# Kernel optimization log

Hardware: AMD Instinct MI355X
Metric: run time of the kernel (lower is better)

The kernel has to match this reference:

```python
import jax, jax.numpy as jnp
import numpy as np

B, NQ, NK, C = 16, 8, 4096, 256
H = W = 64
HEADS = 8
CI = 128          # embedding_dim // attention_downsample_rate
HD = CI // HEADS  # per-head dim
EPS = float(np.finfo(np.float32).tiny)


def _gumbel_topk(scores, noise, n):
    # iterative gumbel-softmax top-k relaxation with straight-through hard k-hot
    g = scores + noise
    khot = jnp.zeros_like(g)
    onehot = jnp.zeros_like(g)
    for _ in range(n):
        g = g + jnp.log(jnp.maximum(1.0 - onehot, EPS))
        onehot = jax.nn.softmax(g, axis=-1)
        khot = khot + onehot
    _, ind = jax.lax.top_k(khot, n)
    rows = jnp.arange(khot.shape[0])[:, None]
    hard = jnp.zeros_like(khot).at[rows, ind].set(1.0)
    ret = hard - jax.lax.stop_gradient(khot) + khot  # == hard numerically
    return ret, jnp.sort(ind, axis=1)  # sorted idx = row-major order of boolean-mask select


def _sample_points(pe, content, ret, idx):
    # pe [H,W,C], content [b,H,W,C], ret [b,HW] k-hot, idx [b,k] sorted
    b = ret.shape[0]
    m = ret.reshape(b, H, W, 1)
    pe_m = (pe[None] * m).reshape(b, H * W, -1)
    c_m = (content * m).reshape(b, H * W, -1)
    take = lambda a: jnp.take_along_axis(a, idx[:, :, None], axis=1)
    return take(pe_m), take(c_m)


def _mlp(x, W1, b1, W2, b2, W3, b3):
    x = jax.nn.relu(x @ W1 + b1)
    x = jax.nn.relu(x @ W2 + b2)
    return x @ W3 + b3


def _forward(queries, keys, query_pe, key_pe, guiding_embedding, gumbel_p, gumbel_n,
             static_uncertain, static_refined, Wq, bq, Wk, bk, Wv, bv, Wo, bo,
             uW1, ub1, uW2, ub2, uW3, ub3, rW1, rb1, rW2, rb2, rW3, rb3,
             pe_gauss, point_pos, point_neg, n_sample_points):
    b = queries.shape[0]
    g = guiding_embedding.reshape(b, C, H * W).transpose(0, 2, 1)  # [b, HW, C]
    g = g * keys  # elementwise gating -> new guiding embedding

    # cross attention token -> image (internal dim CI, HEADS heads)
    def split_heads(x, Wx, bx):
        return (x @ Wx + bx).reshape(b, -1, HEADS, HD).transpose(0, 2, 1, 3)
    qh = split_heads(queries + query_pe, Wq, bq)
    kh = split_heads(g + key_pe, Wk, bk)
    vh = split_heads(g, Wv, bv)
    attn = jax.nn.softmax(jnp.einsum('bhqd,bhkd->bhqk', qh, kh) / np.float32(np.sqrt(HD)), axis=-1)
    out = jnp.einsum('bhqk,bhkd->bhqd', attn, vh).transpose(0, 2, 1, 3).reshape(b, -1, CI)
    queries = out @ Wo + bo  # [b, NQ, C]

    q1 = queries[:, 1, :]
    unc_tok = _mlp(jnp.concatenate([jnp.broadcast_to(static_uncertain, (b, C)), q1], -1),
                   uW1, ub1, uW2, ub2, uW3, ub3)
    ref_tok = _mlp(jnp.concatenate([jnp.broadcast_to(static_refined, (b, C)), q1], -1),
                   rW1, rb1, rW2, rb2, rW3, rb3)

    img = g.transpose(0, 2, 1)  # [b, C, HW]
    unc_norm = jax.nn.sigmoid(jnp.einsum('bc,bcn->bn', unc_tok, img))
    ref_mask = jnp.einsum('bc,bcn->bn', ref_tok, img)
    coarse_mask = jnp.einsum('bc,bcn->bn', q1, img)

    queries = jnp.concatenate([queries[:, 0:1], ref_tok[:, None, :], queries[:, 2:]], axis=1)

    # point-sampling reference map + gumbel-softmax top-k (training-path math)
    ref_map = unc_norm * (jax.nn.sigmoid(ref_mask) - jax.nn.sigmoid(coarse_mask))  # [b, HW]
    ret_p, idx_p = _gumbel_topk(ref_map, gumbel_p, n_sample_points)
    ret_n, idx_n = _gumbel_topk(-ref_map, gumbel_n, n_sample_points)

    # random fourier positional encoding of the 64x64 grid (SAM PositionEmbeddingRandom)
    xs = (jnp.arange(W, dtype=jnp.float32) + 0.5) / W
    ys = (jnp.arange(H, dtype=jnp.float32) + 0.5) / H
    coords = jnp.stack([jnp.tile(xs[None, :], (H, 1)), jnp.tile(ys[:, None], (1, W))], axis=-1)
    proj = ((2.0 * coords - 1.0) @ pe_gauss) * np.float32(2.0 * np.pi)  # [H, W, C//2]
    pe = jnp.concatenate([jnp.sin(proj), jnp.cos(proj)], axis=-1)       # [H, W, C]

    # F.interpolate of a 64x64 map to (64,64) is the identity here
    content = (keys + g).reshape(b, H, W, C)

    sp_pe, sp_c = _sample_points(pe, content, ret_p, idx_p)
    sn_pe, sn_c = _sample_points(pe, content, ret_n, idx_n)
    sp_pe = sp_pe + point_pos  # prompt_encoder.point_embeddings[1]
    sn_pe = sn_pe + point_neg  # prompt_encoder.point_embeddings[0]

    query_pe = jnp.concatenate([query_pe, sp_pe, sn_pe], axis=1)
    queries = jnp.concatenate([queries, sp_c, sn_c], axis=1)
    # pack (queries, query_pe) into one array for a single-output reference
    return jnp.concatenate([queries, query_pe], axis=1)  # [b, 2*(NQ+2k), C]


def setup_inputs():
    key = jax.random.key(0)
    ks = iter(jax.random.split(key, 48))
    n = lambda shape, s=1.0: jax.random.normal(next(ks), shape, jnp.float32) * s
    z = lambda shape: jnp.zeros(shape, jnp.float32)
    return {
        'queries': n((B, NQ, C)),
        'keys': n((B, NK, C)),
        'query_pe': n((B, NQ, C)),
        'key_pe': n((B, NK, C)),
        'guiding_embedding': n((B, C, H, W)),
        'gumbel_p': jax.random.gumbel(next(ks), (B, NK), jnp.float32),
        'gumbel_n': jax.random.gumbel(next(ks), (B, NK), jnp.float32),
        'static_uncertain': n((C,), 0.02),
        'static_refined': n((C,), 0.02),
        'Wq': n((C, CI), 0.02), 'bq': z((CI,)),
        'Wk': n((C, CI), 0.02), 'bk': z((CI,)),
        'Wv': n((C, CI), 0.02), 'bv': z((CI,)),
        'Wo': n((CI, C), 0.02), 'bo': z((C,)),
        'uW1': n((2 * C, C // 4), 0.05), 'ub1': z((C // 4,)),
        'uW2': n((C // 4, C // 4), 0.05), 'ub2': z((C // 4,)),
        'uW3': n((C // 4, C), 0.05), 'ub3': z((C,)),
        'rW1': n((2 * C, C // 4), 0.05), 'rb1': z((C // 4,)),
        'rW2': n((C // 4, C // 4), 0.05), 'rb2': z((C // 4,)),
        'rW3': n((C // 4, C), 0.05), 'rb3': z((C,)),
        'pe_gauss': n((2, C // 2)),
        'point_pos': n((C,), 0.02),
        'point_neg': n((C,), 0.02),
        'n_sample_points': 4,
    }


def reference(queries, keys, query_pe, key_pe, guiding_embedding, gumbel_p, gumbel_n,
              static_uncertain, static_refined, Wq, bq, Wk, bk, Wv, bv, Wo, bo,
              uW1, ub1, uW2, ub2, uW3, ub3, rW1, rb1, rW2, rb2, rW3, rb3,
              pe_gauss, point_pos, point_neg, n_sample_points):
    return _forward(queries, keys, query_pe, key_pe, guiding_embedding, gumbel_p, gumbel_n,
                    static_uncertain, static_refined, Wq, bq, Wk, bk, Wv, bv, Wo, bo,
                    uW1, ub1, uW2, ub2, uW3, ub3, rW1, rb1, rW2, rb2, rW3, rb3,
                    pe_gauss, point_pos, point_neg, n_sample_points)
```

## Files before the change

### kernel.cpp

```cpp
#include <hip/hip_runtime.h>

#define BB 16
#define NQn 8
#define NK 4096
#define CC 256
#define NHEADS 8
#define CIn 128
#define HDn 16
#define NHQ 64
#define EPS_TINY 1.17549435e-38f

constexpr size_t OFF_QK   = 0;
constexpr size_t OFF_QBK  = OFF_QK  + (size_t)BB*CC*NHQ;
constexpr size_t OFF_SC   = OFF_QBK + (size_t)BB*NHQ;
constexpr size_t OFF_MP   = OFF_SC  + (size_t)BB*NK*NHQ;
constexpr size_t OFF_SP   = OFF_MP  + (size_t)BB*16*NHQ;
constexpr size_t OFF_M    = OFF_SP  + (size_t)BB*16*NHQ;
constexpr size_t OFF_RS   = OFF_M   + (size_t)BB*NHQ;
constexpr size_t OFF_AVP  = OFF_RS  + (size_t)BB*NHQ;
constexpr size_t OFF_QATT = OFF_AVP + (size_t)BB*16*NHQ*CC;
constexpr size_t OFF_UNC  = OFF_QATT+ (size_t)BB*NQn*CC;
constexpr size_t OFF_REFT = OFF_UNC + (size_t)BB*CC;
constexpr size_t OFF_RMAP = OFF_REFT+ (size_t)BB*CC;
constexpr size_t OFF_IDX  = OFF_RMAP+ (size_t)BB*NK;
constexpr size_t OFF_RV   = OFF_IDX + 128;
constexpr size_t OFF_G    = OFF_RV  + 128;

__global__ __launch_bounds__(256) void k1_qside(
    const float* __restrict__ queries, const float* __restrict__ query_pe,
    const float* __restrict__ Wq, const float* __restrict__ bq,
    const float* __restrict__ Wk, const float* __restrict__ bk,
    float* __restrict__ ws)
{
  int b = blockIdx.x >> 3, q = blockIdx.x & 7, t = threadIdx.x;
  __shared__ float x[CC];
  __shared__ float qh[CIn];
  x[t] = queries[(b*NQn+q)*CC + t] + query_pe[(b*NQn+q)*CC + t];
  __syncthreads();
  if (t < CIn) {
    float a = bq[t];
    for (int c = 0; c < CC; ++c) a += x[c]*Wq[c*CIn + t];
    qh[t] = a * 0.25f;
  }
  __syncthreads();
  float* Qk = ws + OFF_QK;
  #pragma unroll
  for (int h = 0; h < NHEADS; ++h) {
    float a = 0.f;
    #pragma unroll
    for (int d = 0; d < HDn; ++d) a += qh[h*HDn+d] * Wk[t*CIn + h*HDn + d];
    Qk[((size_t)b*CC + t)*NHQ + h*NQn + q] = a;
  }
  if (t < NHEADS) {
    float a = 0.f;
    #pragma unroll
    for (int d = 0; d < HDn; ++d) a += qh[t*HDn+d] * bk[t*HDn+d];
    (ws + OFF_QBK)[b*NHQ + t*NQn + q] = a;
  }
}

__global__ __launch_bounds__(256) void k2_scores(
    const float* __restrict__ keys, const float* __restrict__ key_pe,
    const float* __restrict__ guiding, float* __restrict__ ws)
{
  int b = blockIdx.y, n0 = blockIdx.x * 64, t = threadIdx.x;
  __shared__ __align__(16) float Xs[64][68];
  __shared__ __align__(16) float Qs[64][64];
  __shared__ float Gt[64][65];
  const float* Qk = ws + OFF_QK;
  float* G = ws + OFF_G;
  int tx = t & 15, ty = t >> 4;
  int c4 = tx*4, rowg = ty;
  int lane = t & 63, grp = t >> 6;
  float acc[4][4] = {};

  float gpref[16];
  float4 kpref[4], ppref[4];
  float qpref[16];
  #pragma unroll
  for (int cc = 0; cc < 16; ++cc)
    gpref[cc] = guiding[((size_t)b*CC + grp*16+cc)*NK + n0 + lane];
  #pragma unroll
  for (int p = 0; p < 4; ++p) {
    size_t base = ((size_t)b*NK + n0 + p*16+rowg)*CC + c4;
    kpref[p] = *(const float4*)&keys[base];
    ppref[p] = *(const float4*)&key_pe[base];
  }
  #pragma unroll
  for (int i = 0; i < 16; ++i) {
    int l = i*256 + t;
    qpref[i] = Qk[((size_t)b*CC + (l>>6))*NHQ + (l & 63)];
  }

  for (int c0 = 0; c0 < CC; c0 += 64) {
    #pragma unroll
    for (int cc = 0; cc < 16; ++cc) Gt[grp*16+cc][lane] = gpref[cc];
    __syncthreads();
    #pragma unroll
    for (int i = 0; i < 16; ++i) {
      int l = i*256 + t;
      Qs[l >> 6][l & 63] = qpref[i];
    }
    #pragma unroll
    for (int p = 0; p < 4; ++p) {
      int row = p*16 + rowg;
      size_t base = ((size_t)b*NK + n0 + row)*CC + c0 + c4;
      float4 kv = kpref[p], pv = ppref[p];
      float4 g4;
      g4.x = kv.x * Gt[c4+0][row];
      g4.y = kv.y * Gt[c4+1][row];
      g4.z = kv.z * Gt[c4+2][row];
      g4.w = kv.w * Gt[c4+3][row];
      *(float4*)&G[base] = g4;
      float4 o; o.x = g4.x+pv.x; o.y = g4.y+pv.y; o.z = g4.z+pv.z; o.w = g4.w+pv.w;
      *(float4*)&Xs[row][c4] = o;
    }
    __syncthreads();
    if (c0 + 64 < CC) {
      int c1 = c0 + 64;
      #pragma unroll
      for (int cc = 0; cc < 16; ++cc)
        gpref[cc] = guiding[((size_t)b*CC + c1 + grp*16+cc)*NK + n0 + lane];
      #pragma unroll
      for (int p = 0; p < 4; ++p) {
        size_t base = ((size_t)b*NK + n0 + p*16+rowg)*CC + c1 + c4;
        kpref[p] = *(const float4*)&keys[base];
        ppref[p] = *(const float4*)&key_pe[base];
      }
      #pragma unroll
      for (int i = 0; i < 16; ++i) {
        int l = i*256 + t;
        qpref[i] = Qk[((size_t)b*CC + c1 + (l>>6))*NHQ + (l & 63)];
      }
    }
    #pragma unroll 4
    for (int cb = 0; cb < 16; ++cb) {
      float4 xf[4], qf[4];
      #pragma unroll
      for (int i = 0; i < 4; ++i) xf[i] = *(const float4*)&Xs[4*ty+i][4*cb];
      #pragma unroll
      for (int u = 0; u < 4; ++u) qf[u] = *(const float4*)&Qs[4*cb+u][4*tx];
      #pragma unroll
      for (int u = 0; u < 4; ++u) {
        float xu[4] = { ((const float*)&xf[0])[u], ((const float*)&xf[1])[u],
                        ((const float*)&xf[2])[u], ((const float*)&xf[3])[u] };
        float qu[4] = { qf[u].x, qf[u].y, qf[u].z, qf[u].w };
        #pragma unroll
        for (int i = 0; i < 4; ++i)
          #pragma unroll
          for (int j = 0; j < 4; ++j) acc[i][j] += xu[i]*qu[j];
      }
    }
  }
  const float* qbk = ws + OFF_QBK + (size_t)b*NHQ;
  float qb[4] = {qbk[4*tx], qbk[4*tx+1], qbk[4*tx+2], qbk[4*tx+3]};
  float* sc = ws + OFF_SC + ((size_t)b*NK + n0)*NHQ;
  #pragma unroll
  for (int i = 0; i < 4; ++i) {
    float4 o;
    o.x = acc[i][0]+qb[0]; o.y = acc[i][1]+qb[1]; o.z = acc[i][2]+qb[2]; o.w = acc[i][3]+qb[3];
    *(float4*)&sc[(4*ty + i)*NHQ + 4*tx] = o;
  }
}

__global__ __launch_bounds__(256) void k3a_stats(float* __restrict__ ws)
{
  int b = blockIdx.y, sb = blockIdx.x, t = threadIdx.x;
  int hq = t & 63, r = t >> 6;
  const float* sc = ws + OFF_SC + ((size_t)b*NK + sb*256)*NHQ;
  float m = -INFINITY, s = 0.f;
  for (int i = 0; i < 64; ++i) {
    float v = sc[(r + 4*i)*NHQ + hq];
    if (v > m) { s = s*expf(m - v) + 1.f; m = v; } else { s += expf(v - m); }
  }
  __shared__ float rm[256], rs[256];
  rm[t] = m; rs[t] = s;
  __syncthreads();
  if (t < 64) {
    float m0=rm[t], m1=rm[t+64], m2=rm[t+128], m3=rm[t+192];
    float mm = fmaxf(fmaxf(m0,m1), fmaxf(m2,m3));
    float ss = rs[t]*expf(m0-mm) + rs[t+64]*expf(m1-mm) + rs[t+128]*expf(m2-mm) + rs[t+192]*expf(m3-mm);
    (ws + OFF_MP)[(b*16 + sb)*NHQ + t] = mm;
    (ws + OFF_SP)[(b*16 + sb)*NHQ + t] = ss;
  }
}

__global__ __launch_bounds__(64) void k3b_combine(float* __restrict__ ws)
{
  int b = blockIdx.x, hq = threadIdx.x;
  const float* mp = ws + OFF_MP + (size_t)b*16*NHQ;
  const float* sp = ws + OFF_SP + (size_t)b*16*NHQ;
  float m = -INFINITY;
  #pragma unroll
  for (int i = 0; i < 16; ++i) m = fmaxf(m, mp[i*NHQ+hq]);
  float s = 0.f;
  #pragma unroll
  for (int i = 0; i < 16; ++i) s += sp[i*NHQ+hq]*expf(mp[i*NHQ+hq]-m);
  (ws+OFF_M)[b*NHQ+hq] = m;
  (ws+OFF_RS)[b*NHQ+hq] = 1.0f/s;
}

__global__ __launch_bounds__(512) void k4_av(float* __restrict__ ws)
{
  int b = blockIdx.y, kb = blockIdx.x, t = threadIdx.x;
  int k0 = kb * 256;
  __shared__ __align__(16) float gld[32][260];
  __shared__ __align__(16) float wld[32][64];
  __shared__ float mv[64], rv[64];
  if (t < 64) { mv[t] = (ws+OFF_M)[b*NHQ+t]; rv[t] = (ws+OFF_RS)[b*NHQ+t]; }
  int hq0 = (t & 7) * 8, c0 = (t >> 3) * 4;
  float accf[8][4] = {};
  const float* sc = ws + OFF_SC;
  const float* G  = ws + OFF_G;
  float4 gpref[4]; float spref[4];
  #pragma unroll
  for (int p = 0; p < 4; ++p) {
    int row = p*8 + (t>>6);
    gpref[p] = *(const float4*)&G[((size_t)b*NK + k0 + row)*CC + (t&63)*4];
  }
  #pragma unroll
  for (int i = 0; i < 4; ++i) {
    int l = i*512 + t;
    spref[i] = sc[((size_t)b*NK + k0 + (l>>6))*NHQ + (l&63)];
  }
  __syncthreads();
  for (int kk = 0; kk < 256; kk += 32) {
    #pragma unroll
    for (int p = 0; p < 4; ++p) {
      int row = p*8 + (t>>6);
      *(float4*)&gld[row][(t&63)*4] = gpref[p];
    }
    #pragma unroll
    for (int i = 0; i < 4; ++i) {
      int l = i*512 + t; int k = l >> 6, hq = l & 63;
      wld[k][hq] = expf(spref[i] - mv[hq]) * rv[hq];
    }
    __syncthreads();
    if (kk + 32 < 256) {
      #pragma unroll
      for (int p = 0; p < 4; ++p) {
        int row = p*8 + (t>>6);
        gpref[p] = *(const float4*)&G[((size_t)b*NK + k0 + kk+32 + row)*CC + (t&63)*4];
      }
      #pragma unroll
      for (int i = 0; i < 4; ++i) {
        int l = i*512 + t;
        spref[i] = sc[((size_t)b*NK + k0 + kk+32 + (l>>6))*NHQ + (l&63)];
      }
    }
    #pragma unroll 2
    for (int k = 0; k < 32; ++k) {
      float4 w0 = *(const float4*)&wld[k][hq0];
      float4 w1 = *(const float4*)&wld[k][hq0+4];
      float4 gv = *(const float4*)&gld[k][c0];
      float wq[8] = {w0.x,w0.y,w0.z,w0.w, w1.x,w1.y,w1.z,w1.w};
      float gq[4] = {gv.x,gv.y,gv.z,gv.w};
      #pragma unroll
      for (int i = 0; i < 8; ++i)
        #pragma unroll
        for (int j = 0; j < 4; ++j) accf[i][j] += wq[i]*gq[j];
    }
    __syncthreads();
  }
  float* avp = ws + OFF_AVP + (((size_t)b*16 + kb)*NHQ)*CC;
  #pragma unroll
  for (int i = 0; i < 8; ++i) {
    float4 o;
    o.x = accf[i][0]; o.y = accf[i][1]; o.z = accf[i][2]; o.w = accf[i][3];
    *(float4*)&avp[(size_t)(hq0 + i)*CC + c0] = o;
  }
}

__global__ __launch_bounds__(256) void k56_attout(
    const float* __restrict__ Wv, const float* __restrict__ bv,
    const float* __restrict__ Wo, const float* __restrict__ bo,
    float* __restrict__ ws)
{
  int b = blockIdx.x >> 3, q = blockIdx.x & 7, t = threadIdx.x;
  __shared__ float avs[NHEADS][CC];
  __shared__ float outv[CIn];
  const float* avp = ws + OFF_AVP;
  #pragma unroll
  for (int h = 0; h < NHEADS; ++h) {
    int hq = h*NQn + q;
    float a = 0.f;
    #pragma unroll 4
    for (int kb = 0; kb < 16; ++kb)
      a += avp[(((size_t)b*16 + kb)*NHQ + hq)*CC + t];
    avs[h][t] = a;
  }
  __syncthreads();
  if (t < CIn) {
    int h = t >> 4;
    float a = bv[t];
    for (int c = 0; c < CC; ++c) a += avs[h][c]*Wv[c*CIn + t];
    outv[t] = a;
  }
  __syncthreads();
  float a = bo[t];
  for (int ci = 0; ci < CIn; ++ci) a += outv[ci]*Wo[ci*CC + t];
  (ws+OFF_QATT)[((size_t)b*NQn + q)*CC + t] = a;
}

__global__ __launch_bounds__(256) void k7_mlps(
    const float* __restrict__ su, const float* __restrict__ sr,
    const float* __restrict__ uW1, const float* __restrict__ ub1,
    const float* __restrict__ uW2, const float* __restrict__ ub2,
    const float* __restrict__ uW3, const float* __restrict__ ub3,
    const float* __restrict__ rW1, const float* __restrict__ rb1,
    const float* __restrict__ rW2, const float* __restrict__ rb2,
    const float* __restrict__ rW3, const float* __restrict__ rb3,
    float* __restrict__ ws)
{
  int b = blockIdx.x, t = threadIdx.x;
  __shared__ float xs[768];
  __shared__ float h1[2][64], h2[2][64];
  xs[t] = su[t];
  xs[256+t] = (ws+OFF_QATT)[((size_t)b*NQn + 1)*CC + t];
  xs[512+t] = sr[t];
  __syncthreads();
  if (t < 128) {
    int which = t >> 6, o = t & 63;
    const float* W1 = which ? rW1 : uW1;
    const float* b1 = which ? rb1 : ub1;
    int base = which ? 512 : 0;
    float a = b1[o];
    for (int i = 0; i < 256; ++i) a += xs[base+i]*W1[i*64 + o];
    for (int i = 0; i < 256; ++i) a += xs[256+i]*W1[(256+i)*64 + o];
    h1[which][o] = fmaxf(a, 0.f);
  }
  __syncthreads();
  if (t < 128) {
    int which = t >> 6, o = t & 63;
    const float* W2 = which ? rW2 : uW2;
    const float* b2 = which ? rb2 : ub2;
    float a = b2[o];
    #pragma unroll 8
    for (int i = 0; i < 64; ++i) a += h1[which][i]*W2[i*64+o];
    h2[which][o] = fmaxf(a, 0.f);
  }
  __syncthreads();
  {
    float a = ub3[t];
    #pragma unroll 8
    for (int i = 0; i < 64; ++i) a += h2[0][i]*uW3[i*CC + t];
    (ws+OFF_UNC)[b*CC + t] = a;
    float a2 = rb3[t];
    #pragma unroll 8
    for (int i = 0; i < 64; ++i) a2 += h2[1][i]*rW3[i*CC + t];
    (ws+OFF_REFT)[b*CC + t] = a2;
  }
}

__global__ __launch_bounds__(256) void k8_masks(float* __restrict__ ws)
{
  int b = blockIdx.y, t = threadIdx.x;
  int wave = t >> 6, lane = t & 63;
  __shared__ float q1s[CC], us[CC], rts[CC];
  q1s[t] = (ws+OFF_QATT)[((size_t)b*NQn+1)*CC + t];
  us[t]  = (ws+OFF_UNC)[b*CC + t];
  rts[t] = (ws+OFF_REFT)[b*CC + t];
  __syncthreads();
  float q1v[4], usv[4], rtv[4];
  #pragma unroll
  for (int u = 0; u < 4; ++u) {
    q1v[u] = q1s[lane*4+u]; usv[u] = us[lane*4+u]; rtv[u] = rts[lane*4+u];
  }
  const float* G = ws + OFF_G;
  float* rmap = ws + OFF_RMAP + (size_t)b*NK;
  int n_base = blockIdx.x*64 + wave*16;
  for (int r = 0; r < 16; ++r) {
    int n = n_base + r;
    float4 gv = *(const float4*)&G[((size_t)b*NK + n)*CC + lane*4];
    float aq = gv.x*q1v[0] + gv.y*q1v[1] + gv.z*q1v[2] + gv.w*q1v[3];
    float au = gv.x*usv[0] + gv.y*usv[1] + gv.z*usv[2] + gv.w*usv[3];
    float ar = gv.x*rtv[0] + gv.y*rtv[1] + gv.z*rtv[2] + gv.w*rtv[3];
    #pragma unroll
    for (int s = 1; s < 64; s <<= 1) {
      aq += __shfl_xor(aq, s, 64);
      au += __shfl_xor(au, s, 64);
      ar += __shfl_xor(ar, s, 64);
    }
    if (lane == 0) {
      float un = 1.f/(1.f+expf(-au));
      rmap[n] = un * (1.f/(1.f+expf(-ar)) - 1.f/(1.f+expf(-aq)));
    }
  }
}

__global__ __launch_bounds__(256) void k9_gumbel(
    const float* __restrict__ gp, const float* __restrict__ gn,
    float* __restrict__ ws)
{
  int sign = blockIdx.x, b = blockIdx.y, t = threadIdx.x;
  int wave = t >> 6, lane = t & 63;
  const float* noise = sign ? gn : gp;
  const float* rmap = ws + OFF_RMAP + (size_t)b*NK;
  float g[16], kh[16], oh[16];
  #pragma unroll
  for (int i = 0; i < 16; ++i) {
    int n = i*256 + t;
    float scv = rmap[n];
    if (sign) scv = -scv;
    g[i] = scv + noise[(size_t)b*NK + n];
    kh[i] = 0.f; oh[i] = 0.f;
  }
  __shared__ float wred[8];
  __shared__ float selV[16];
  __shared__ int   selIdx[16];
  for (int it = 0; it < 4; ++it) {
    if (it > 0) {
      #pragma unroll
      for (int i = 0; i < 16; ++i) g[i] += logf(fmaxf(1.f - oh[i], EPS_TINY));
    }
    float m = g[0];
    #pragma unroll
    for (int i = 1; i < 16; ++i) m = fmaxf(m, g[i]);
    #pragma unroll
    for (int s = 1; s < 64; s <<= 1) m = fmaxf(m, __shfl_xor(m, s, 64));
    if (lane == 0) wred[wave] = m;
    __syncthreads();
    m = fmaxf(fmaxf(wred[0], wred[1]), fmaxf(wred[2], wred[3]));
    float e[16], ls = 0.f;
    #pragma unroll
    for (int i = 0; i < 16; ++i) { e[i] = expf(g[i]-m); ls += e[i]; }
    #pragma unroll
    for (int s = 1; s < 64; s <<= 1) ls += __shfl_xor(ls, s, 64);
    if (lane == 0) wred[4+wave] = ls;
    __syncthreads();
    float ssum = wred[4]+wred[5]+wred[6]+wred[7];
    #pragma unroll
    for (int i = 0; i < 16; ++i) { oh[i] = e[i]/ssum; kh[i] += oh[i]; }
  }
  int id[4]; float rr[4];
  for (int j = 0; j < 4; ++j) {
    float bv = kh[0]; int bi = t;
    #pragma unroll
    for (int i = 1; i < 16; ++i) {
      if (kh[i] > bv) { bv = kh[i]; bi = i*256 + t; }
    }
    #pragma unroll
    for (int s = 1; s < 64; s <<= 1) {
      float ov = __shfl_xor(bv, s, 64);
      int   oi = __shfl_xor(bi, s, 64);
      if (ov > bv || (ov == bv && oi < bi)) { bv = ov; bi = oi; }
    }
    if (lane == 0) { selV[j*4+wave] = bv; selIdx[j*4+wave] = bi; }
    __syncthreads();
    bv = selV[j*4]; bi = selIdx[j*4];
    #pragma unroll
    for (int w = 1; w < 4; ++w) {
      float ov = selV[j*4+w]; int oi = selIdx[j*4+w];
      if (ov > bv || (ov == bv && oi < bi)) { bv = ov; bi = oi; }
    }
    id[j] = bi; rr[j] = (1.f - bv) + bv;
    if ((bi & 255) == t) kh[bi >> 8] = -1.f;
  }
  if (t == 0) {
    for (int a = 0; a < 3; ++a)
      for (int c2 = a+1; c2 < 4; ++c2)
        if (id[c2] < id[a]) { int ti=id[a]; id[a]=id[c2]; id[c2]=ti; float tr=rr[a]; rr[a]=rr[c2]; rr[c2]=tr; }
    int* iout = (int*)(ws + OFF_IDX);
    float* rout = ws + OFF_RV;
    for (int j = 0; j < 4; ++j) {
      iout[(sign*BB + b)*4 + j] = id[j];
      rout[(sign*BB + b)*4 + j] = rr[j];
    }
  }
}

__global__ __launch_bounds__(256) void k10_out(
    const float* __restrict__ keys, const float* __restrict__ query_pe,
    const float* __restrict__ point_pos, const float* __restrict__ point_neg,
    const float* __restrict__ pe_gauss,
    float* __restrict__ ws, float* __restrict__ out)
{
  int b = blockIdx.y, r = blockIdx.x, t = threadIdx.x;
  const float* G = ws + OFF_G;
  float val;
  if (r < 8) {
    val = (r == 1) ? (ws+OFF_REFT)[b*CC + t]
                   : (ws+OFF_QATT)[((size_t)b*NQn + r)*CC + t];
  } else if (r < 16) {
    int j = r - 8; int sign = j >> 2; int jj = j & 3;
    int idx = ((const int*)(ws+OFF_IDX))[(sign*BB + b)*4 + jj];
    float rvv = (ws+OFF_RV)[(sign*BB + b)*4 + jj];
    float kv = keys[((size_t)b*NK + idx)*CC + t];
    float gv = G[((size_t)b*NK + idx)*CC + t];
    val = (kv + gv) * rvv;
  } else if (r < 24) {
    val = query_pe[((size_t)b*NQn + (r-16))*CC + t];
  } else {
    int j = r - 24; int sign = j >> 2; int jj = j & 3;
    int idx = ((const int*)(ws+OFF_IDX))[(sign*BB + b)*4 + jj];
    float rvv = (ws+OFF_RV)[(sign*BB + b)*4 + jj];
    const float* point = sign ? point_neg : point_pos;
    int h = idx >> 6, w = idx & 63;
    float x = (w + 0.5f)/64.f, y = (h + 0.5f)/64.f;
    int jf = (t < 128) ? t : (t - 128);
    float proj = ((2.f*x - 1.f)*pe_gauss[jf] + (2.f*y - 1.f)*pe_gauss[128 + jf]) * 6.28318530717958647692f;
    float sv = (t < 128) ? sinf(proj) : cosf(proj);
    val = sv*rvv + point[t];
  }
  out[((size_t)b*32 + r)*CC + t] = val;
}

extern "C" void kernel_launch(void* const* d_in, const int* in_sizes, int n_in,
                              void* d_out, int out_size, void* d_ws, size_t ws_size,
                              hipStream_t stream)
{
  const float* queries   = (const float*)d_in[0];
  const float* keys      = (const float*)d_in[1];
  const float* query_pe  = (const float*)d_in[2];
  const float* key_pe    = (const float*)d_in[3];
  const float* guiding   = (const float*)d_in[4];
  const float* gumbel_p  = (const float*)d_in[5];
  const float* gumbel_n  = (const float*)d_in[6];
  const float* s_unc     = (const float*)d_in[7];
  const float* s_ref     = (const float*)d_in[8];
  const float* Wq  = (const float*)d_in[9];   const float* bq  = (const float*)d_in[10];
  const float* Wk  = (const float*)d_in[11];  const float* bk  = (const float*)d_in[12];
  const float* Wv  = (const float*)d_in[13];  const float* bv  = (const float*)d_in[14];
  const float* Wo  = (const float*)d_in[15];  const float* bo  = (const float*)d_in[16];
  const float* uW1 = (const float*)d_in[17];  const float* ub1 = (const float*)d_in[18];
  const float* uW2 = (const float*)d_in[19];  const float* ub2 = (const float*)d_in[20];
  const float* uW3 = (const float*)d_in[21];  const float* ub3 = (const float*)d_in[22];
  const float* rW1 = (const float*)d_in[23];  const float* rb1 = (const float*)d_in[24];
  const float* rW2 = (const float*)d_in[25];  const float* rb2 = (const float*)d_in[26];
  const float* rW3 = (const float*)d_in[27];  const float* rb3 = (const float*)d_in[28];
  const float* pe_gauss  = (const float*)d_in[29];
  const float* point_pos = (const float*)d_in[30];
  const float* point_neg = (const float*)d_in[31];
  float* ws = (float*)d_ws;
  float* out = (float*)d_out;

  k1_qside  <<<dim3(BB*NQn),  256, 0, stream>>>(queries, query_pe, Wq, bq, Wk, bk, ws);
  k2_scores <<<dim3(64, BB),  256, 0, stream>>>(keys, key_pe, guiding, ws);
  k3a_stats <<<dim3(16, BB),  256, 0, stream>>>(ws);
  k3b_combine<<<dim3(BB),      64, 0, stream>>>(ws);
  k4_av     <<<dim3(16, BB),  512, 0, stream>>>(ws);
  k56_attout<<<dim3(BB*NQn),  256, 0, stream>>>(Wv, bv, Wo, bo, ws);
  k7_mlps   <<<dim3(BB),      256, 0, stream>>>(s_unc, s_ref, uW1, ub1, uW2, ub2, uW3, ub3,
                                                rW1, rb1, rW2, rb2, rW3, rb3, ws);
  k8_masks  <<<dim3(64, BB),  256, 0, stream>>>(ws);
  k9_gumbel <<<dim3(2, BB),   256, 0, stream>>>(gumbel_p, gumbel_n, ws);
  k10_out   <<<dim3(32, BB),  256, 0, stream>>>(keys, query_pe, point_pos, point_neg,
                                                pe_gauss, ws, out);
}
```

Baseline: 243.3 us.

## Drop k2 register prefetch and Q smem tile; split k4 across channel halves

In k2_scores, the register-level software prefetch of guiding, keys, key_pe and Qk is removed. The Qs shared tile is dropped and Qk is read directly from global memory (L1/L2) inside the inner product loop, which shrinks LDS use and register pressure at the cost of exposed load latency. In k4_av, the grid gains a channel-half dimension so each block handles 128 channels with a 4x4 register tile instead of 8x4. This doubles the block count for more occupancy and parallelism but reloads the score tiles twice.

Measured after the change: 330.3 us. 35.7% more time.

```diff
diff --git a/kernel.cpp b/kernel.cpp
--- a/kernel.cpp
+++ b/kernel.cpp
@@ -64,48 +64,29 @@
     const float* __restrict__ guiding, float* __restrict__ ws)
 {
   int b = blockIdx.y, n0 = blockIdx.x * 64, t = threadIdx.x;
-  __shared__ __align__(16) float Xs[64][68];
-  __shared__ __align__(16) float Qs[64][64];
+  __shared__ __align__(16) float Xs[64][66];
   __shared__ float Gt[64][65];
-  const float* Qk = ws + OFF_QK;
+  const float* Qk = ws + OFF_QK + (size_t)b*CC*NHQ;
   float* G = ws + OFF_G;
   int tx = t & 15, ty = t >> 4;
   int c4 = tx*4, rowg = ty;
   int lane = t & 63, grp = t >> 6;
   float acc[4][4] = {};
 
-  float gpref[16];
-  float4 kpref[4], ppref[4];
-  float qpref[16];
-  #pragma unroll
-  for (int cc = 0; cc < 16; ++cc)
-    gpref[cc] = guiding[((size_t)b*CC + grp*16+cc)*NK + n0 + lane];
-  #pragma unroll
-  for (int p = 0; p < 4; ++p) {
-    size_t base = ((size_t)b*NK + n0 + p*16+rowg)*CC + c4;
-    kpref[p] = *(const float4*)&keys[base];
-    ppref[p] = *(const float4*)&key_pe[base];
-  }
-  #pragma unroll
-  for (int i = 0; i < 16; ++i) {
-    int l = i*256 + t;
-    qpref[i] = Qk[((size_t)b*CC + (l>>6))*NHQ + (l & 63)];
-  }
-
   for (int c0 = 0; c0 < CC; c0 += 64) {
-    #pragma unroll
-    for (int cc = 0; cc < 16; ++cc) Gt[grp*16+cc][lane] = gpref[cc];
-    __syncthreads();
-    #pragma unroll
-    for (int i = 0; i < 16; ++i) {
-      int l = i*256 + t;
-      Qs[l >> 6][l & 63] = qpref[i];
-    }
+    __syncthreads();
+    #pragma unroll
+    for (int cc = 0; cc < 16; ++cc) {
+      int c = grp*16 + cc;
+      Gt[c][lane] = guiding[((size_t)b*CC + c0 + c)*NK + n0 + lane];
+    }
+    __syncthreads();
     #pragma unroll
     for (int p = 0; p < 4; ++p) {
       int row = p*16 + rowg;
       size_t base = ((size_t)b*NK + n0 + row)*CC + c0 + c4;
-      float4 kv = kpref[p], pv = ppref[p];
+      float4 kv = *(const float4*)&keys[base];
+      float4 pv = *(const float4*)&key_pe[base];
       float4 g4;
       g4.x = kv.x * Gt[c4+0][row];
       g4.y = kv.y * Gt[c4+1][row];
@@ -116,35 +97,17 @@
       *(float4*)&Xs[row][c4] = o;
     }
     __syncthreads();
-    if (c0 + 64 < CC) {
-      int c1 = c0 + 64;
-      #pragma unroll
-      for (int cc = 0; cc < 16; ++cc)
-        gpref[cc] = guiding[((size_t)b*CC + c1 + grp*16+cc)*NK + n0 + lane];
-      #pragma unroll
-      for (int p = 0; p < 4; ++p) {
-        size_t base = ((size_t)b*NK + n0 + p*16+rowg)*CC + c1 + c4;
-        kpref[p] = *(const float4*)&keys[base];
-        ppref[p] = *(const float4*)&key_pe[base];
-      }
-      #pragma unroll
-      for (int i = 0; i < 16; ++i) {
-        int l = i*256 + t;
-        qpref[i] = Qk[((size_t)b*CC + c1 + (l>>6))*NHQ + (l & 63)];
-      }
-    }
     #pragma unroll 4
     for (int cb = 0; cb < 16; ++cb) {
-      float4 xf[4], qf[4];
+      float4 xf[4];
       #pragma unroll
       for (int i = 0; i < 4; ++i) xf[i] = *(const float4*)&Xs[4*ty+i][4*cb];
       #pragma unroll
-      for (int u = 0; u < 4; ++u) qf[u] = *(const float4*)&Qs[4*cb+u][4*tx];
-      #pragma unroll
       for (int u = 0; u < 4; ++u) {
+        float4 qf = *(const float4*)&Qk[(size_t)(c0 + 4*cb + u)*NHQ + 4*tx];
         float xu[4] = { ((const float*)&xf[0])[u], ((const float*)&xf[1])[u],
                         ((const float*)&xf[2])[u], ((const float*)&xf[3])[u] };
-        float qu[4] = { qf[u].x, qf[u].y, qf[u].z, qf[u].w };
+        float qu[4] = { qf.x, qf.y, qf.z, qf.w };
         #pragma unroll
         for (int i = 0; i < 4; ++i)
           #pragma unroll
@@ -202,22 +165,21 @@
 
 __global__ __launch_bounds__(512) void k4_av(float* __restrict__ ws)
 {
-  int b = blockIdx.y, kb = blockIdx.x, t = threadIdx.x;
-  int k0 = kb * 256;
-  __shared__ __align__(16) float gld[32][260];
+  int kb = blockIdx.x, ch = blockIdx.y, b = blockIdx.z, t = threadIdx.x;
+  int k0 = kb * 256, cbase = ch * 128;
+  __shared__ __align__(16) float gld[32][132];
   __shared__ __align__(16) float wld[32][64];
   __shared__ float mv[64], rv[64];
   if (t < 64) { mv[t] = (ws+OFF_M)[b*NHQ+t]; rv[t] = (ws+OFF_RS)[b*NHQ+t]; }
-  int hq0 = (t & 7) * 8, c0 = (t >> 3) * 4;
-  float accf[8][4] = {};
+  int hq0 = (t & 15) * 4, c0 = (t >> 4) * 4;
+  int srow = t >> 5, sc4 = (t & 31) * 4;
+  float accf[4][4] = {};
   const float* sc = ws + OFF_SC;
   const float* G  = ws + OFF_G;
-  float4 gpref[4]; float spref[4];
-  #pragma unroll
-  for (int p = 0; p < 4; ++p) {
-    int row = p*8 + (t>>6);
-    gpref[p] = *(const float4*)&G[((size_t)b*NK + k0 + row)*CC + (t&63)*4];
-  }
+  float4 gpref[2]; float spref[4];
+  #pragma unroll
+  for (int p = 0; p < 2; ++p)
+    gpref[p] = *(const float4*)&G[((size_t)b*NK + k0 + p*16 + srow)*CC + cbase + sc4];
   #pragma unroll
   for (int i = 0; i < 4; ++i) {
     int l = i*512 + t;
@@ -226,10 +188,8 @@
   __syncthreads();
   for (int kk = 0; kk < 256; kk += 32) {
     #pragma unroll
-    for (int p = 0; p < 4; ++p) {
-      int row = p*8 + (t>>6);
-      *(float4*)&gld[row][(t&63)*4] = gpref[p];
-    }
+    for (int p = 0; p < 2; ++p)
+      *(float4*)&gld[p*16 + srow][sc4] = gpref[p];
     #pragma unroll
     for (int i = 0; i < 4; ++i) {
       int l = i*512 + t; int k = l >> 6, hq = l & 63;
@@ -238,25 +198,22 @@
     __syncthreads();
     if (kk + 32 < 256) {
       #pragma unroll
-      for (int p = 0; p < 4; ++p) {
-        int row = p*8 + (t>>6);
-        gpref[p] = *(const float4*)&G[((size_t)b*NK + k0 + kk+32 + row)*CC + (t&63)*4];
-      }
+      for (int p = 0; p < 2; ++p)
+        gpref[p] = *(const float4*)&G[((size_t)b*NK + k0 + kk+32 + p*16 + srow)*CC + cbase + sc4];
       #pragma unroll
       for (int i = 0; i < 4; ++i) {
         int l = i*512 + t;
         spref[i] = sc[((size_t)b*NK + k0 + kk+32 + (l>>6))*NHQ + (l&63)];
       }
     }
-    #pragma unroll 2
+    #pragma unroll 4
     for (int k = 0; k < 32; ++k) {
-      float4 w0 = *(const float4*)&wld[k][hq0];
-      float4 w1 = *(const float4*)&wld[k][hq0+4];
+      float4 w4 = *(const float4*)&wld[k][hq0];
       float4 gv = *(const float4*)&gld[k][c0];
-      float wq[8] = {w0.x,w0.y,w0.z,w0.w, w1.x,w1.y,w1.z,w1.w};
-      float gq[4] = {gv.x,gv.y,gv.z,gv.w};
+      float wq[4] = {w4.x, w4.y, w4.z, w4.w};
+      float gq[4] = {gv.x, gv.y, gv.z, gv.w};
       #pragma unroll
-      for (int i = 0; i < 8; ++i)
+      for (int i = 0; i < 4; ++i)
         #pragma unroll
         for (int j = 0; j < 4; ++j) accf[i][j] += wq[i]*gq[j];
     }
@@ -264,10 +221,10 @@
   }
   float* avp = ws + OFF_AVP + (((size_t)b*16 + kb)*NHQ)*CC;
   #pragma unroll
-  for (int i = 0; i < 8; ++i) {
+  for (int i = 0; i < 4; ++i) {
     float4 o;
     o.x = accf[i][0]; o.y = accf[i][1]; o.z = accf[i][2]; o.w = accf[i][3];
-    *(float4*)&avp[(size_t)(hq0 + i)*CC + c0] = o;
+    *(float4*)&avp[(size_t)(hq0 + i)*CC + cbase + c0] = o;
   }
 }
 
@@ -534,16 +491,16 @@
   float* ws = (float*)d_ws;
   float* out = (float*)d_out;
 
-  k1_qside  <<<dim3(BB*NQn),  256, 0, stream>>>(queries, query_pe, Wq, bq, Wk, bk, ws);
-  k2_scores <<<dim3(64, BB),  256, 0, stream>>>(keys, key_pe, guiding, ws);
-  k3a_stats <<<dim3(16, BB),  256, 0, stream>>>(ws);
-  k3b_combine<<<dim3(BB),      64, 0, stream>>>(ws);
-  k4_av     <<<dim3(16, BB),  512, 0, stream>>>(ws);
-  k56_attout<<<dim3(BB*NQn),  256, 0, stream>>>(Wv, bv, Wo, bo, ws);
-  k7_mlps   <<<dim3(BB),      256, 0, stream>>>(s_unc, s_ref, uW1, ub1, uW2, ub2, uW3, ub3,
-                                                rW1, rb1, rW2, rb2, rW3, rb3, ws);
-  k8_masks  <<<dim3(64, BB),  256, 0, stream>>>(ws);
-  k9_gumbel <<<dim3(2, BB),   256, 0, stream>>>(gumbel_p, gumbel_n, ws);
-  k10_out   <<<dim3(32, BB),  256, 0, stream>>>(keys, query_pe, point_pos, point_neg,
-                                                pe_gauss, ws, out);
-}
+  k1_qside  <<<dim3(BB*NQn),    256, 0, stream>>>(queries, query_pe, Wq, bq, Wk, bk, ws);
+  k2_scores <<<dim3(64, BB),    256, 0, stream>>>(keys, key_pe, guiding, ws);
+  k3a_stats <<<dim3(16, BB),    256, 0, stream>>>(ws);
+  k3b_combine<<<dim3(BB),        64, 0, stream>>>(ws);
+  k4_av     <<<dim3(16, 2, BB), 512, 0, stream>>>(ws);
+  k56_attout<<<dim3(BB*NQn),    256, 0, stream>>>(Wv, bv, Wo, bo, ws);
+  k7_mlps   <<<dim3(BB),        256, 0, stream>>>(s_unc, s_ref, uW1, ub1, uW2, ub2, uW3, ub3,
+                                                  rW1, rb1, rW2, rb2, rW3, rb3, ws);
+  k8_masks  <<<dim3(64, BB),    256, 0, stream>>>(ws);
+  k9_gumbel <<<dim3(2, BB),     256, 0, stream>>>(gumbel_p, gumbel_n, ws);
+  k10_out   <<<dim3(32, BB),    256, 0, stream>>>(keys, query_pe, point_pos, point_neg,
+                                                  pe_gauss, ws, out);
+}
```
